# Kernel optimization log

Measured on AMD Instinct MI355X. Metric: run time of the kernel, lower is better.

Reference implementation:

```python
import jax, jax.numpy as jnp
import numpy as np

DIM_IN = 1024
DIM_OUT = 1024
B = 8192


def setup_inputs() -> dict:
    key = jax.random.key(0)
    ks = jax.random.split(key, 8)
    d = DIM_IN + DIM_OUT
    bound = 1.0 / np.sqrt(d)
    def lin(kw, kb):
        W = jax.random.uniform(kw, (d, DIM_OUT), jnp.float32, -bound, bound)
        b = jax.random.uniform(kb, (DIM_OUT,), jnp.float32, -bound, bound)
        return W, b
    kx, kh, kc, kp = ks[0], ks[1], ks[2], ks[3]
    pw = jax.random.split(kp, 8)
    W_I, b_I = lin(pw[0], pw[1])
    W_F, b_F = lin(pw[2], pw[3])
    W_G, b_G = lin(pw[4], pw[5])
    W_O, b_O = lin(pw[6], pw[7])
    return {
        "x": jax.random.normal(kx, (B, DIM_IN), jnp.float32),
        "h": jax.random.normal(kh, (B, DIM_OUT), jnp.float32),
        "c": jax.random.normal(kc, (B, DIM_OUT), jnp.float32),
        "W_I": W_I, "b_I": b_I,
        "W_F": W_F, "b_F": b_F,
        "W_G": W_G, "b_G": b_G,
        "W_O": W_O, "b_O": b_O,
    }


def reference(x, h, c, W_I, b_I, W_F, b_F, W_G, b_G, W_O, b_O):
    X = jnp.concatenate([x, h], axis=-1)  # [B, dimIn+dimOut]
    # Fuse the 4 gate projections into one GEMM: [B,d] @ [d, 4*dimOut]
    W = jnp.concatenate([W_I, W_F, W_G, W_O], axis=1)
    b = jnp.concatenate([b_I, b_F, b_G, b_O], axis=0)
    gates = X @ W + b
    i_, f_, g_, o_ = jnp.split(gates, 4, axis=-1)
    I = jax.nn.sigmoid(i_)
    F = jax.nn.sigmoid(f_)
    G = jnp.tanh(g_)
    O = jax.nn.sigmoid(o_)
    C = F * c + I * G
    return O * jnp.tanh(C), C
```

## Files before the change

kernel.cpp:

```cpp
#include <hip/hip_runtime.h>
#include <cstdint>


#define B_ROWS 8192
#define DK 2048
#define DOUT 1024
#define BM 256
#define BN 256
#define BK 64
#define NKT (DK / BK)

typedef __bf16 bf16x8 __attribute__((ext_vector_type(8)));
typedef __bf16 bf16x4 __attribute__((ext_vector_type(4)));
typedef float f32x16 __attribute__((ext_vector_type(16)));

__device__ inline void load16_to_lds(const __bf16* gsrc, __bf16* ldst) {
    __builtin_amdgcn_global_load_lds(
        (const __attribute__((address_space(1))) void*)gsrc,
        (__attribute__((address_space(3))) void*)ldst,
        16, 0, 0);
}

__device__ inline float fast_sigmoid(float x) {
    return __builtin_amdgcn_rcpf(1.0f + __builtin_amdgcn_exp2f(-1.442695041f * x));
}
__device__ inline float fast_tanh(float x) {
    return 1.0f - 2.0f * __builtin_amdgcn_rcpf(1.0f + __builtin_amdgcn_exp2f(2.885390082f * x));
}

__global__ __launch_bounds__(256) void prep_all(
    const float* __restrict__ x, const float* __restrict__ h,
    __bf16* __restrict__ X,
    const float* __restrict__ WI, const float* __restrict__ WF,
    const float* __restrict__ WG, const float* __restrict__ WO,
    __bf16* __restrict__ Wt)
{
    __shared__ float t[32][33];
    if (blockIdx.x >= 2048) {
        int id = (blockIdx.x - 2048) * 256 + threadIdx.x;
        int b = id >> 9;
        int k = (id & 511) * 4;
        float4 v;
        if (k < 1024) v = *(const float4*)&x[(size_t)b * 1024 + k];
        else          v = *(const float4*)&h[(size_t)b * 1024 + (k - 1024)];
        bf16x4 o = { (__bf16)v.x, (__bf16)v.y, (__bf16)v.z, (__bf16)v.w };
        *(bf16x4*)&X[(size_t)b * 2048 + k] = o;
        return;
    }
    int kb = blockIdx.x & 63;
    int jb = blockIdx.x >> 6;
    int j0 = jb * 32;
    int tx = threadIdx.x & 31, ty = threadIdx.x >> 5;
    const float* Ws[4] = {WI, WF, WG, WO};
#pragma unroll
    for (int g = 0; g < 4; ++g) {
        const float* W = Ws[g];
#pragma unroll
        for (int yy = 0; yy < 32; yy += 8) {
            int k = kb * 32 + ty + yy;
            t[ty + yy][tx] = W[(size_t)k * 1024 + j0 + tx];
        }
        __syncthreads();
#pragma unroll
        for (int yy = 0; yy < 32; yy += 8) {
            int r = ty + yy;
            int npp = jb * 128 + g * 32 + r;
            Wt[(size_t)npp * 2048 + kb * 32 + tx] = (__bf16)t[tx][r];
        }
        __syncthreads();
    }
}

__global__ __launch_bounds__(512, 2) void lstm_gemm(
    const __bf16* __restrict__ Xbf, const __bf16* __restrict__ Wt,
    const float* __restrict__ c,
    const float* __restrict__ bI, const float* __restrict__ bF,
    const float* __restrict__ bG, const float* __restrict__ bO,
    float* __restrict__ outH, float* __restrict__ outC)
{
    __shared__ __bf16 lds[2][2][2][8192];

    const int tid  = threadIdx.x;
    const int lane = tid & 63;
    const int wave = tid >> 6;
    const int wm = wave >> 1;
    const int wn = wave & 1;

    const int bid = blockIdx.x;
    const int id  = (bid & 7) * 64 + (bid >> 3);
    const int mb = id & 31;
    const int nb = id >> 5;
    const int m0 = mb * BM;
    const int n0 = nb * BN;

    const int c0 = wave >> 2;
    const int r0 = (wave & 3) * 64 + lane;
    const __bf16* gA0 = Xbf + (size_t)(m0 + r0) * DK + c0 * 8;
    const __bf16* gA1 = Xbf + (size_t)(m0 + r0) * DK + (c0 + 2) * 8;
    const __bf16* gB0 = Wt  + (size_t)(n0 + r0) * DK + c0 * 8;
    const __bf16* gB1 = Wt  + (size_t)(n0 + r0) * DK + (c0 + 2) * 8;
    const int ls0 = wave * 512;
    const int ls1 = ls0 + 4096;

    const int lr = lane & 31;
    const int kq = lane >> 5;
    int aoff[2][2], boff[4][2];
#pragma unroll
    for (int mi = 0; mi < 2; ++mi) {
        int row = wm * 64 + mi * 32 + lr;
#pragma unroll
        for (int ks = 0; ks < 2; ++ks)
            aoff[mi][ks] = ((2 * ks + kq) * 256 + row) * 8;
    }
#pragma unroll
    for (int nf = 0; nf < 4; ++nf) {
        int row = wn * 128 + nf * 32 + lr;
#pragma unroll
        for (int ks = 0; ks < 2; ++ks)
            boff[nf][ks] = ((2 * ks + kq) * 256 + row) * 8;
    }

    f32x16 acc[2][4];
#pragma unroll
    for (int mi = 0; mi < 2; ++mi)
#pragma unroll
        for (int nf = 0; nf < 4; ++nf)
#pragma unroll
            for (int e = 0; e < 16; ++e) acc[mi][nf][e] = 0.f;

#define STAGE_A(d_, kh_, ko_) do { \
    load16_to_lds(gA0 + (ko_) + (kh_) * 32, &lds[d_][0][kh_][ls0]); \
    load16_to_lds(gA1 + (ko_) + (kh_) * 32, &lds[d_][0][kh_][ls1]); } while (0)
#define STAGE_B(d_, kh_, ko_) do { \
    load16_to_lds(gB0 + (ko_) + (kh_) * 32, &lds[d_][1][kh_][ls0]); \
    load16_to_lds(gB1 + (ko_) + (kh_) * 32, &lds[d_][1][kh_][ls1]); } while (0)

#define PHASE(d_, dn_, kh_, ko_, vm_, st_) do { \
    asm volatile("s_waitcnt " vm_ " lgkmcnt(0)" ::: "memory"); \
    __builtin_amdgcn_s_barrier(); \
    asm volatile("" ::: "memory"); \
    bf16x8 a0_  = *(const bf16x8*)&lds[d_][0][kh_][aoff[0][0]]; \
    bf16x8 b0_  = *(const bf16x8*)&lds[d_][1][kh_][boff[0][0]]; \
    bf16x8 b1_  = *(const bf16x8*)&lds[d_][1][kh_][boff[1][0]]; \
    bf16x8 b2_  = *(const bf16x8*)&lds[d_][1][kh_][boff[2][0]]; \
    bf16x8 b3_  = *(const bf16x8*)&lds[d_][1][kh_][boff[3][0]]; \
    bf16x8 a1_  = *(const bf16x8*)&lds[d_][0][kh_][aoff[1][0]]; \
    bf16x8 a0k_ = *(const bf16x8*)&lds[d_][0][kh_][aoff[0][1]]; \
    bf16x8 b0k_ = *(const bf16x8*)&lds[d_][1][kh_][boff[0][1]]; \
    bf16x8 b1k_ = *(const bf16x8*)&lds[d_][1][kh_][boff[1][1]]; \
    bf16x8 b2k_ = *(const bf16x8*)&lds[d_][1][kh_][boff[2][1]]; \
    bf16x8 b3k_ = *(const bf16x8*)&lds[d_][1][kh_][boff[3][1]]; \
    bf16x8 a1k_ = *(const bf16x8*)&lds[d_][0][kh_][aoff[1][1]]; \
    if (st_) { STAGE_A(dn_, kh_, ko_); STAGE_B(dn_, kh_, ko_); } \
    __builtin_amdgcn_s_setprio(1); \
    acc[0][0] = __builtin_amdgcn_mfma_f32_32x32x16_bf16(a0_, b0_, acc[0][0], 0, 0, 0); \
    acc[0][1] = __builtin_amdgcn_mfma_f32_32x32x16_bf16(a0_, b1_, acc[0][1], 0, 0, 0); \
    acc[0][2] = __builtin_amdgcn_mfma_f32_32x32x16_bf16(a0_, b2_, acc[0][2], 0, 0, 0); \
    acc[0][3] = __builtin_amdgcn_mfma_f32_32x32x16_bf16(a0_, b3_, acc[0][3], 0, 0, 0); \
    acc[1][0] = __builtin_amdgcn_mfma_f32_32x32x16_bf16(a1_, b0_, acc[1][0], 0, 0, 0); \
    acc[1][1] = __builtin_amdgcn_mfma_f32_32x32x16_bf16(a1_, b1_, acc[1][1], 0, 0, 0); \
    acc[1][2] = __builtin_amdgcn_mfma_f32_32x32x16_bf16(a1_, b2_, acc[1][2], 0, 0, 0); \
    acc[1][3] = __builtin_amdgcn_mfma_f32_32x32x16_bf16(a1_, b3_, acc[1][3], 0, 0, 0); \
    acc[0][0] = __builtin_amdgcn_mfma_f32_32x32x16_bf16(a0k_, b0k_, acc[0][0], 0, 0, 0); \
    acc[0][1] = __builtin_amdgcn_mfma_f32_32x32x16_bf16(a0k_, b1k_, acc[0][1], 0, 0, 0); \
    acc[0][2] = __builtin_amdgcn_mfma_f32_32x32x16_bf16(a0k_, b2k_, acc[0][2], 0, 0, 0); \
    acc[0][3] = __builtin_amdgcn_mfma_f32_32x32x16_bf16(a0k_, b3k_, acc[0][3], 0, 0, 0); \
    acc[1][0] = __builtin_amdgcn_mfma_f32_32x32x16_bf16(a1k_, b0k_, acc[1][0], 0, 0, 0); \
    acc[1][1] = __builtin_amdgcn_mfma_f32_32x32x16_bf16(a1k_, b1k_, acc[1][1], 0, 0, 0); \
    acc[1][2] = __builtin_amdgcn_mfma_f32_32x32x16_bf16(a1k_, b2k_, acc[1][2], 0, 0, 0); \
    acc[1][3] = __builtin_amdgcn_mfma_f32_32x32x16_bf16(a1k_, b3k_, acc[1][3], 0, 0, 0); \
    __builtin_amdgcn_s_setprio(0); \
} while (0)

    STAGE_A(0, 0, 0);
    STAGE_B(0, 0, 0);
    STAGE_A(0, 1, 0);
    STAGE_B(0, 1, 0);

    for (int t = 0; t < NKT - 2; t += 2) {
        const int ko0 = (t + 1) * BK;
        const int ko1 = (t + 2) * BK;
        PHASE(0, 1, 0, ko0, "vmcnt(4)", 1);
        PHASE(0, 1, 1, ko0, "vmcnt(4)", 1);
        PHASE(1, 0, 0, ko1, "vmcnt(4)", 1);
        PHASE(1, 0, 1, ko1, "vmcnt(4)", 1);
    }
    PHASE(0, 1, 0, (NKT - 1) * BK, "vmcnt(4)", 1);
    PHASE(0, 1, 1, (NKT - 1) * BK, "vmcnt(4)", 1);
    PHASE(1, 0, 0, 0, "vmcnt(4)", 0);
    PHASE(1, 0, 1, 0, "vmcnt(0)", 0);

#undef PHASE
#undef STAGE_A
#undef STAGE_B

    const int j = (nb * 2 + wn) * 32 + lr;
    const float biI = bI[j], biF = bF[j], biG = bG[j], biO = bO[j];
    const int rb = m0 + wm * 64 + 4 * kq;
#pragma unroll
    for (int mi = 0; mi < 2; ++mi) {
#pragma unroll
        for (int rg = 0; rg < 16; ++rg) {
            int row = rb + mi * 32 + (rg & 3) + 8 * (rg >> 2);
            float I = fast_sigmoid(acc[mi][0][rg] + biI);
            float F = fast_sigmoid(acc[mi][1][rg] + biF);
            float G = fast_tanh(acc[mi][2][rg] + biG);
            float O = fast_sigmoid(acc[mi][3][rg] + biO);
            size_t idx = (size_t)row * DOUT + j;
            float Cn = F * c[idx] + I * G;
            outH[idx] = O * fast_tanh(Cn);
            outC[idx] = Cn;
        }
    }
}

extern "C" void kernel_launch(void* const* d_in, const int* in_sizes, int n_in,
                              void* d_out, int out_size, void* d_ws, size_t ws_size,
                              hipStream_t stream) {
    const float* x  = (const float*)d_in[0];
    const float* h  = (const float*)d_in[1];
    const float* c  = (const float*)d_in[2];
    const float* WI = (const float*)d_in[3];
    const float* bI = (const float*)d_in[4];
    const float* WF = (const float*)d_in[5];
    const float* bF = (const float*)d_in[6];
    const float* WG = (const float*)d_in[7];
    const float* bG = (const float*)d_in[8];
    const float* WO = (const float*)d_in[9];
    const float* bO = (const float*)d_in[10];

    __bf16* Xbf = (__bf16*)d_ws;
    __bf16* Wt  = (__bf16*)((char*)d_ws + (size_t)B_ROWS * DK * 2);
    float* outH = (float*)d_out;
    float* outC = outH + (size_t)B_ROWS * DOUT;

    prep_all<<<2048 + (B_ROWS * DK / 4) / 256, 256, 0, stream>>>(
        x, h, Xbf, WI, WF, WG, WO, Wt);
    lstm_gemm<<<dim3((B_ROWS / BM) * (4 * DOUT / BN)), dim3(512), 0, stream>>>(
        Xbf, Wt, c, bI, bF, bG, bO, outH, outC);
}
```

Baseline: 384.9 us.

## Pre-tile X and W into LDS-ready contiguous chunks for GEMM staging

The prep kernel now writes X and the transposed weights in a tiled layout, where each 64-wide K half-tile of a 256-row block is one contiguous 16 KB chunk in the exact order the GEMM's LDS staging expects. The GEMM's global-to-LDS loads then read fully contiguous memory instead of strided row segments. The weight prep also drops the shared-memory transpose and instead gathers 8 strided scalar reads per thread, which may make that part less coalesced.

```diff
diff --git a/kernel.cpp b/kernel.cpp
--- a/kernel.cpp
+++ b/kernel.cpp
@@ -11,7 +11,6 @@
 #define NKT (DK / BK)
 
 typedef __bf16 bf16x8 __attribute__((ext_vector_type(8)));
-typedef __bf16 bf16x4 __attribute__((ext_vector_type(4)));
 typedef float f32x16 __attribute__((ext_vector_type(16)));
 
 __device__ inline void load16_to_lds(const __bf16* gsrc, __bf16* ldst) {
@@ -30,49 +29,52 @@
 
 __global__ __launch_bounds__(256) void prep_all(
     const float* __restrict__ x, const float* __restrict__ h,
-    __bf16* __restrict__ X,
+    __bf16* __restrict__ Xt,
     const float* __restrict__ WI, const float* __restrict__ WF,
     const float* __restrict__ WG, const float* __restrict__ WO,
-    __bf16* __restrict__ Wt)
+    __bf16* __restrict__ Wtt)
 {
-    __shared__ float t[32][33];
-    if (blockIdx.x >= 2048) {
-        int id = (blockIdx.x - 2048) * 256 + threadIdx.x;
-        int b = id >> 9;
-        int k = (id & 511) * 4;
-        float4 v;
-        if (k < 1024) v = *(const float4*)&x[(size_t)b * 1024 + k];
-        else          v = *(const float4*)&h[(size_t)b * 1024 + (k - 1024)];
-        bf16x4 o = { (__bf16)v.x, (__bf16)v.y, (__bf16)v.z, (__bf16)v.w };
-        *(bf16x4*)&X[(size_t)b * 2048 + k] = o;
-        return;
-    }
-    int kb = blockIdx.x & 63;
-    int jb = blockIdx.x >> 6;
-    int j0 = jb * 32;
-    int tx = threadIdx.x & 31, ty = threadIdx.x >> 5;
-    const float* Ws[4] = {WI, WF, WG, WO};
-#pragma unroll
-    for (int g = 0; g < 4; ++g) {
-        const float* W = Ws[g];
-#pragma unroll
-        for (int yy = 0; yy < 32; yy += 8) {
-            int k = kb * 32 + ty + yy;
-            t[ty + yy][tx] = W[(size_t)k * 1024 + j0 + tx];
+    const int tid = threadIdx.x;
+    if (blockIdx.x < 1024) {
+        const int u  = blockIdx.x;
+        const int nt = u >> 6, kt = (u >> 1) & 31, kh = u & 1;
+        const float* Ws[4] = {WI, WF, WG, WO};
+        __bf16* dst = Wtt + (size_t)u * 8192;
+        const int k0 = kt * 64 + kh * 32;
+#pragma unroll
+        for (int ii = 0; ii < 4; ++ii) {
+            int gi = ii * 256 + tid;
+            int cc = gi >> 8, r = gi & 255;
+            int g  = (r >> 5) & 3;
+            int j  = (nt * 2 + (r >> 7)) * 32 + (r & 31);
+            const float* W = Ws[g] + (size_t)(k0 + cc * 8) * 1024 + j;
+            bf16x8 o;
+#pragma unroll
+            for (int e = 0; e < 8; ++e) o[e] = (__bf16)W[(size_t)e * 1024];
+            *(bf16x8*)&dst[(size_t)gi * 8] = o;
         }
-        __syncthreads();
-#pragma unroll
-        for (int yy = 0; yy < 32; yy += 8) {
-            int r = ty + yy;
-            int npp = jb * 128 + g * 32 + r;
-            Wt[(size_t)npp * 2048 + kb * 32 + tx] = (__bf16)t[tx][r];
+    } else {
+        const int u  = blockIdx.x - 1024;
+        const int mt = u >> 6, kt = (u >> 1) & 31, kh = u & 1;
+        const float* src = (kt < 16) ? x : h;
+        const int kbase = kt * 64 + kh * 32 - (kt < 16 ? 0 : 1024);
+        __bf16* dst = Xt + (size_t)u * 8192;
+#pragma unroll
+        for (int ii = 0; ii < 4; ++ii) {
+            int gi = ii * 256 + tid;
+            int cc = gi >> 8, r = gi & 255;
+            const float* s = src + (size_t)(mt * 256 + r) * 1024 + kbase + cc * 8;
+            float4 v0 = *(const float4*)s;
+            float4 v1 = *(const float4*)(s + 4);
+            bf16x8 o = {(__bf16)v0.x, (__bf16)v0.y, (__bf16)v0.z, (__bf16)v0.w,
+                        (__bf16)v1.x, (__bf16)v1.y, (__bf16)v1.z, (__bf16)v1.w};
+            *(bf16x8*)&dst[(size_t)gi * 8] = o;
         }
-        __syncthreads();
     }
 }
 
 __global__ __launch_bounds__(512, 2) void lstm_gemm(
-    const __bf16* __restrict__ Xbf, const __bf16* __restrict__ Wt,
+    const __bf16* __restrict__ Xt, const __bf16* __restrict__ Wtt,
     const float* __restrict__ c,
     const float* __restrict__ bI, const float* __restrict__ bF,
     const float* __restrict__ bG, const float* __restrict__ bO,
@@ -91,14 +93,10 @@
     const int mb = id & 31;
     const int nb = id >> 5;
     const int m0 = mb * BM;
-    const int n0 = nb * BN;
-
-    const int c0 = wave >> 2;
-    const int r0 = (wave & 3) * 64 + lane;
-    const __bf16* gA0 = Xbf + (size_t)(m0 + r0) * DK + c0 * 8;
-    const __bf16* gA1 = Xbf + (size_t)(m0 + r0) * DK + (c0 + 2) * 8;
-    const __bf16* gB0 = Wt  + (size_t)(n0 + r0) * DK + c0 * 8;
-    const __bf16* gB1 = Wt  + (size_t)(n0 + r0) * DK + (c0 + 2) * 8;
+
+    const int s = wave * 64 + lane;
+    const __bf16* gA = Xt  + (size_t)(mb * NKT * 2) * 8192 + (size_t)s * 8;
+    const __bf16* gB = Wtt + (size_t)(nb * NKT * 2) * 8192 + (size_t)s * 8;
     const int ls0 = wave * 512;
     const int ls1 = ls0 + 4096;
 
@@ -128,14 +126,16 @@
 #pragma unroll
             for (int e = 0; e < 16; ++e) acc[mi][nf][e] = 0.f;
 
-#define STAGE_A(d_, kh_, ko_) do { \
-    load16_to_lds(gA0 + (ko_) + (kh_) * 32, &lds[d_][0][kh_][ls0]); \
-    load16_to_lds(gA1 + (ko_) + (kh_) * 32, &lds[d_][0][kh_][ls1]); } while (0)
-#define STAGE_B(d_, kh_, ko_) do { \
-    load16_to_lds(gB0 + (ko_) + (kh_) * 32, &lds[d_][1][kh_][ls0]); \
-    load16_to_lds(gB1 + (ko_) + (kh_) * 32, &lds[d_][1][kh_][ls1]); } while (0)
-
-#define PHASE(d_, dn_, kh_, ko_, vm_, st_) do { \
+#define STAGE_A(d_, kh_, t_) do { \
+    const __bf16* pa_ = gA + (((t_) * 2 + (kh_)) << 13); \
+    load16_to_lds(pa_, &lds[d_][0][kh_][ls0]); \
+    load16_to_lds(pa_ + 4096, &lds[d_][0][kh_][ls1]); } while (0)
+#define STAGE_B(d_, kh_, t_) do { \
+    const __bf16* pb_ = gB + (((t_) * 2 + (kh_)) << 13); \
+    load16_to_lds(pb_, &lds[d_][1][kh_][ls0]); \
+    load16_to_lds(pb_ + 4096, &lds[d_][1][kh_][ls1]); } while (0)
+
+#define PHASE(d_, dn_, kh_, tn_, vm_, st_) do { \
     asm volatile("s_waitcnt " vm_ " lgkmcnt(0)" ::: "memory"); \
     __builtin_amdgcn_s_barrier(); \
     asm volatile("" ::: "memory"); \
@@ -151,7 +151,7 @@
     bf16x8 b2k_ = *(const bf16x8*)&lds[d_][1][kh_][boff[2][1]]; \
     bf16x8 b3k_ = *(const bf16x8*)&lds[d_][1][kh_][boff[3][1]]; \
     bf16x8 a1k_ = *(const bf16x8*)&lds[d_][0][kh_][aoff[1][1]]; \
-    if (st_) { STAGE_A(dn_, kh_, ko_); STAGE_B(dn_, kh_, ko_); } \
+    if (st_) { STAGE_A(dn_, kh_, tn_); STAGE_B(dn_, kh_, tn_); } \
     __builtin_amdgcn_s_setprio(1); \
     acc[0][0] = __builtin_amdgcn_mfma_f32_32x32x16_bf16(a0_, b0_, acc[0][0], 0, 0, 0); \
     acc[0][1] = __builtin_amdgcn_mfma_f32_32x32x16_bf16(a0_, b1_, acc[0][1], 0, 0, 0); \
@@ -178,15 +178,13 @@
     STAGE_B(0, 1, 0);
 
     for (int t = 0; t < NKT - 2; t += 2) {
-        const int ko0 = (t + 1) * BK;
-        const int ko1 = (t + 2) * BK;
-        PHASE(0, 1, 0, ko0, "vmcnt(4)", 1);
-        PHASE(0, 1, 1, ko0, "vmcnt(4)", 1);
-        PHASE(1, 0, 0, ko1, "vmcnt(4)", 1);
-        PHASE(1, 0, 1, ko1, "vmcnt(4)", 1);
-    }
-    PHASE(0, 1, 0, (NKT - 1) * BK, "vmcnt(4)", 1);
-    PHASE(0, 1, 1, (NKT - 1) * BK, "vmcnt(4)", 1);
+        PHASE(0, 1, 0, t + 1, "vmcnt(4)", 1);
+        PHASE(0, 1, 1, t + 1, "vmcnt(4)", 1);
+        PHASE(1, 0, 0, t + 2, "vmcnt(4)", 1);
+        PHASE(1, 0, 1, t + 2, "vmcnt(4)", 1);
+    }
+    PHASE(0, 1, 0, NKT - 1, "vmcnt(4)", 1);
+    PHASE(0, 1, 1, NKT - 1, "vmcnt(4)", 1);
     PHASE(1, 0, 0, 0, "vmcnt(4)", 0);
     PHASE(1, 0, 1, 0, "vmcnt(0)", 0);
 
@@ -229,13 +227,12 @@
     const float* WO = (const float*)d_in[9];
     const float* bO = (const float*)d_in[10];
 
-    __bf16* Xbf = (__bf16*)d_ws;
-    __bf16* Wt  = (__bf16*)((char*)d_ws + (size_t)B_ROWS * DK * 2);
+    __bf16* Xt  = (__bf16*)d_ws;
+    __bf16* Wtt = (__bf16*)((char*)d_ws + (size_t)B_ROWS * DK * 2);
     float* outH = (float*)d_out;
     float* outC = outH + (size_t)B_ROWS * DOUT;
 
-    prep_all<<<2048 + (B_ROWS * DK / 4) / 256, 256, 0, stream>>>(
-        x, h, Xbf, WI, WF, WG, WO, Wt);
+    prep_all<<<3072, 256, 0, stream>>>(x, h, Xt, WI, WF, WG, WO, Wtt);
     lstm_gemm<<<dim3((B_ROWS / BM) * (4 * DOUT / BN)), dim3(512), 0, stream>>>(
-        Xbf, Wt, c, bI, bF, bG, bO, outH, outC);
-}
+        Xt, Wtt, c, bI, bF, bG, bO, outH, outC);
+}
```

Result: faster. 315.5 us (-18.0%).
